# Performance work log

Measured on AMD Instinct MI355X. Metric: run time of the kernel, lower is better.

The kernel has to match this reference:

```python
import jax, jax.numpy as jnp
import numpy as np

NUM_TOKENS = 14
DIM = 128
B, N = 8, 128
NUM_ROUNDS = 5


def setup_inputs() -> dict:
    key = jax.random.key(0)
    ks = jax.random.split(key, 10)
    s = 1.0 / np.sqrt(DIM)
    return {
        "tok": jax.random.randint(ks[0], (B, N), 0, NUM_TOKENS),
        "A": jax.random.uniform(ks[1], (B, N, N), dtype=jnp.float32),
        "embed": jax.random.normal(ks[2], (NUM_TOKENS, DIM), dtype=jnp.float32),
        "W1": jax.random.normal(ks[3], (DIM, 2 * DIM), dtype=jnp.float32) * s,
        "b1": jax.random.normal(ks[4], (DIM,), dtype=jnp.float32) * s,
        "W2": jax.random.normal(ks[5], (DIM, DIM), dtype=jnp.float32) * s,
        "b2": jax.random.normal(ks[6], (DIM,), dtype=jnp.float32) * s,
        "Wo1": jax.random.normal(ks[7], (DIM, DIM), dtype=jnp.float32) * s,
        "bo1": jax.random.normal(ks[8], (DIM,), dtype=jnp.float32) * s,
        "Wo2": jax.random.normal(ks[9], (10, DIM), dtype=jnp.float32) * s,
    }


def reference(tok, A, embed, W1, b1, W2, b2, Wo1, bo1, Wo2):
    # Dropout is identity (eval mode / inference reference).
    x = embed[tok]  # [B, N, D]
    d = x.shape[-1]
    # fc1 on concat(x_i, x_j) decomposes into two per-node projections:
    # fc1([x_i, x_j]) = x_i @ W1a^T + x_j @ W1b^T + b1
    W1a, W1b = W1[:, :d], W1[:, d:]
    A_t = jnp.swapaxes(A, 1, 2)  # A.transpose(1, 2)
    for _ in range(NUM_ROUNDS):
        hi = jnp.einsum("bnd,ed->bne", x, W1a)
        hj = jnp.einsum("bnd,ed->bne", x, W1b)
        # pairwise edge MLP: [B, N, N, D]
        h = jax.nn.relu(hi[:, :, None, :] + hj[:, None, :, :] + b1)
        m = jax.nn.relu(jnp.einsum("bijd,ed->bije", h, W2) + b2)
        # mask by transposed adjacency and sum over neighbors j (axis 2)
        msg = jnp.einsum("bij,bije->bie", A_t, m)
        x = x + msg
    def head(z):
        return jax.nn.relu(z @ Wo1.T + bo1) @ Wo2.T
    out = head(x[:, 0, :])                       # [B, 10]
    x_all = head(x.reshape(-1, d)).reshape(x.shape[0], x.shape[1], 10)
    return (out, x_all)
```

## Files before the change

### kernel.cpp

```cpp
#include <hip/hip_runtime.h>
#include <hip/hip_bf16.h>

#define BB 8
#define NN 128
#define DD 128

typedef __attribute__((ext_vector_type(8))) short bf16x8;
typedef __attribute__((ext_vector_type(4))) float floatx4;
typedef __attribute__((ext_vector_type(2))) float floatx2;

__device__ __forceinline__ unsigned short f2bf(float f) {
    unsigned int bits = __float_as_uint(f);
    unsigned int r = bits + 0x7FFFu + ((bits >> 16) & 1u);
    return (unsigned short)(r >> 16);
}

__device__ __forceinline__ unsigned short f2bf_hw(float f) {
    unsigned int r;
    asm("v_cvt_pk_bf16_f32 %0, %1, %2" : "=v"(r) : "v"(f), "v"(f));
    return (unsigned short)r;
}

__device__ __forceinline__ unsigned int f2bf_pk(float lo, float hi) {
    unsigned int r;
    asm("v_cvt_pk_bf16_f32 %0, %1, %2" : "=v"(r) : "v"(lo), "v"(hi));
    return r;
}

#define WS_X16A 0
#define WS_X16B 65536
#define WS_W1T  131072
#define WS_W2B  148480
#define WS_CNT  157184

__global__ __launch_bounds__(256) void k_init(const int* __restrict__ tok,
                                              const float* __restrict__ embf,
                                              const float* __restrict__ W1f,
                                              const float* __restrict__ W2f,
                                              float* __restrict__ ws) {
    unsigned int* x16 = (unsigned int*)(ws + WS_X16A);
    unsigned short* gw1t = (unsigned short*)(ws + WS_W1T);
    unsigned short* gw2b = (unsigned short*)(ws + WS_W2B);
    int* cnt = (int*)(ws + WS_CNT);
    int blk = blockIdx.x, t = threadIdx.x;
    if (blk < 16) {
        int base = blk * 4096;
#pragma unroll
        for (int it = 0; it < 16; ++it) {
            int w = base + it * 256 + t;
            int r = w >> 6, d2 = (w & 63) * 2;
            const float* er = embf + tok[r] * DD;
            x16[w] = (unsigned int)f2bf(er[d2]) | ((unsigned int)f2bf(er[d2 + 1]) << 16);
        }
    } else if (blk < 25) {
        int base = (blk - 16) * 4096;
#pragma unroll
        for (int it = 0; it < 16; ++it) {
            int idx = base + it * 256 + t;
            if (idx < 256 * 136) {
                int e = idx / 136, d = idx - e * 136;
                gw1t[idx] = (d < 128) ? f2bf(W1f[(e & 127) * 256 + (e >> 7) * 128 + d])
                                      : (unsigned short)0;
            }
        }
    } else if (blk < 30) {
        int base = (blk - 25) * 4096;
#pragma unroll
        for (int it = 0; it < 16; ++it) {
            int idx = base + it * 256 + t;
            if (idx < 128 * 136) {
                int e = idx / 136, d = idx - e * 136;
                gw2b[idx] = (d < 128) ? f2bf(W2f[e * 128 + d]) : (unsigned short)0;
            }
        }
    } else if (blk == 30) {
#pragma unroll
        for (int it = 0; it < 4; ++it) cnt[it * 256 + t] = 0;
    }
}

__global__ __launch_bounds__(512, 2) void k_main(const int* __restrict__ tokp,
                                                 const float* __restrict__ embf,
                                                 const float* __restrict__ Af,
                                                 const float* __restrict__ b1f,
                                                 const float* __restrict__ b2f,
                                                 const float* __restrict__ Wo1f,
                                                 const float* __restrict__ bo1f,
                                                 const float* __restrict__ Wo2f,
                                                 float* __restrict__ ws,
                                                 float* __restrict__ outp) {
    __shared__ __align__(16) unsigned short w1t[256 * 136];
    __shared__ __align__(16) unsigned short w2b[128 * 136];
    __shared__ __align__(16) unsigned short xb[128 * 136];
    __shared__ __align__(16) float red[4][4][128];
    __shared__ __align__(16) float zs[4][128];
    __shared__ float a_s[4][128];
    __shared__ __align__(16) float hja_s[4][128];
    __shared__ float b1s[128], b2s[128];

    const unsigned short* gw1t = (const unsigned short*)(ws + WS_W1T);
    const unsigned short* gw2b = (const unsigned short*)(ws + WS_W2B);
    int* cnt = (int*)(ws + WS_CNT);

    int blk = blockIdx.x;
    int b = blk & 7, g = blk >> 3, i0 = g * 4;
    int t = threadIdx.x;
    int wave = t >> 6, lane = t & 63;
    int col = lane & 15, quad = lane >> 4;

    {
        const uint4* s1 = (const uint4*)gw1t; uint4* d1 = (uint4*)w1t;
#pragma unroll
        for (int it = 0; it < 9; ++it) { int idx = it * 512 + t; if (idx < 4352) d1[idx] = s1[idx]; }
        const uint4* s2 = (const uint4*)gw2b; uint4* d2 = (uint4*)w2b;
#pragma unroll
        for (int it = 0; it < 5; ++it) { int idx = it * 512 + t; if (idx < 2176) d2[idx] = s2[idx]; }
    }
    if (t < 128) { b1s[t] = b1f[t]; b2s[t] = b2f[t]; }
    a_s[t >> 7][t & 127] = Af[(b * NN + (t & 127)) * NN + i0 + (t >> 7)];

    float xown = embf[tokp[b * NN + i0 + (t >> 7)] * DD + (t & 127)];

    const int myw = g >> 2;
    const int qr  = g & 3;

    __syncthreads();

    for (int r = 0; r < 5; ++r) {
        const unsigned short* cur16 = (const unsigned short*)(ws + ((r & 1) ? WS_X16B : WS_X16A));
        unsigned short* nxt16 = (unsigned short*)(ws + ((r & 1) ? WS_X16A : WS_X16B));

        {
            const bf16x8* gp = reinterpret_cast<const bf16x8*>(
                cur16 + (size_t)(b * NN + wave * 16) * DD);
            bf16x8 v0, v1, v2, v3;
            const bf16x8* pl = gp + lane;
            asm volatile(
                "global_load_dwordx4 %0, %4, off sc0 sc1\n\t"
                "global_load_dwordx4 %1, %4, off offset:1024 sc0 sc1\n\t"
                "global_load_dwordx4 %2, %4, off offset:2048 sc0 sc1\n\t"
                "global_load_dwordx4 %3, %4, off offset:3072 sc0 sc1\n\t"
                "s_waitcnt vmcnt(0)"
                : "=&v"(v0), "=&v"(v1), "=&v"(v2), "=&v"(v3)
                : "v"(pl)
                : "memory");
            int r16 = lane >> 4, c8 = (lane & 15) * 8;
            *reinterpret_cast<bf16x8*>(&xb[(wave * 16 + r16     ) * 136 + c8]) = v0;
            *reinterpret_cast<bf16x8*>(&xb[(wave * 16 + r16 + 4 ) * 136 + c8]) = v1;
            *reinterpret_cast<bf16x8*>(&xb[(wave * 16 + r16 + 8 ) * 136 + c8]) = v2;
            *reinterpret_cast<bf16x8*>(&xb[(wave * 16 + r16 + 12) * 136 + c8]) = v3;
            __threadfence_block();
        }

        bf16x8 af[4];
#pragma unroll
        for (int ks = 0; ks < 4; ++ks)
            af[ks] = *reinterpret_cast<const bf16x8*>(&xb[(wave * 16 + col) * 136 + ks * 32 + quad * 8]);
        floatx4 acc1[16];
#pragma unroll
        for (int nt = 8; nt < 16; ++nt) acc1[nt] = (floatx4){0.f, 0.f, 0.f, 0.f};
#pragma unroll
        for (int nt = 8; nt < 16; ++nt)
#pragma unroll
            for (int ks = 0; ks < 4; ++ks) {
                bf16x8 bfc = *reinterpret_cast<const bf16x8*>(&w1t[(nt * 16 + col) * 136 + ks * 32 + quad * 8]);
                acc1[nt] = __builtin_amdgcn_mfma_f32_16x16x32_bf16(af[ks], bfc, acc1[nt], 0, 0, 0);
            }
        if (wave == myw) {
#pragma unroll
            for (int nt = 0; nt < 8; ++nt) acc1[nt] = (floatx4){0.f, 0.f, 0.f, 0.f};
#pragma unroll
            for (int nt = 0; nt < 8; ++nt)
#pragma unroll
                for (int ks = 0; ks < 4; ++ks) {
                    bf16x8 bfc = *reinterpret_cast<const bf16x8*>(&w1t[(nt * 16 + col) * 136 + ks * 32 + quad * 8]);
                    acc1[nt] = __builtin_amdgcn_mfma_f32_16x16x32_bf16(af[ks], bfc, acc1[nt], 0, 0, 0);
                }
            if (quad == qr) {
#pragma unroll
                for (int nt = 0; nt < 8; ++nt) {
                    int d = nt * 16 + col;
#pragma unroll
                    for (int rr = 0; rr < 4; ++rr) hja_s[rr][d] = acc1[nt][rr];
                }
            }
        }
#pragma unroll
        for (int nt = 8; nt < 16; ++nt) {
            int d = (nt - 8) * 16 + col;
#pragma unroll
            for (int rr = 0; rr < 4; ++rr) {
                int j = wave * 16 + quad * 4 + rr;
                xb[j * 136 + d] = f2bf_hw(acc1[nt][rr] + b1s[d]);
            }
        }
        __syncthreads();

        int we = wave & 1, wj = wave >> 1;
        int ebase = we * 64, jbase = wj * 32;
        bf16x8 bw[4][4];
#pragma unroll
        for (int et = 0; et < 4; ++et)
#pragma unroll
            for (int ks = 0; ks < 4; ++ks)
                bw[et][ks] = *reinterpret_cast<const bf16x8*>(&w2b[(ebase + et * 16 + col) * 136 + ks * 32 + quad * 8]);

        floatx2 hjc[2][4][4];
#pragma unroll
        for (int jt = 0; jt < 2; ++jt)
#pragma unroll
            for (int ks = 0; ks < 4; ++ks) {
                union { bf16x8 v; unsigned int u[4]; } Rw;
                Rw.v = *reinterpret_cast<const bf16x8*>(&xb[(jbase + jt * 16 + col) * 136 + ks * 32 + quad * 8]);
#pragma unroll
                for (int p = 0; p < 4; ++p) {
                    floatx2 h2;
                    h2.x = __uint_as_float(Rw.u[p] << 16);
                    h2.y = __uint_as_float(Rw.u[p] & 0xFFFF0000u);
                    hjc[jt][ks][p] = h2;
                }
            }

#pragma unroll
        for (int ii = 0; ii < 4; ++ii) {
            floatx4 acc2[2][4];
#pragma unroll
            for (int jt = 0; jt < 2; ++jt)
#pragma unroll
                for (int et = 0; et < 4; ++et) acc2[jt][et] = (floatx4){0.f, 0.f, 0.f, 0.f};
#pragma unroll
            for (int ks = 0; ks < 4; ++ks) {
                int k0 = ks * 32 + quad * 8;
                floatx2 ha[4];
#pragma unroll
                for (int p = 0; p < 4; ++p)
                    ha[p] = *reinterpret_cast<const floatx2*>(&hja_s[ii][k0 + 2 * p]);
#pragma unroll
                for (int jt = 0; jt < 2; ++jt) {
                    union { bf16x8 v; unsigned int u[4]; } Ho;
#pragma unroll
                    for (int p = 0; p < 4; ++p) {
                        floatx2 s2;
                        asm("v_pk_add_f32 %0, %1, %2" : "=v"(s2) : "v"(hjc[jt][ks][p]), "v"(ha[p]));
                        float f0 = fmaxf(s2.x, 0.f);
                        float f1 = fmaxf(s2.y, 0.f);
                        Ho.u[p] = f2bf_pk(f0, f1);
                    }
#pragma unroll
                    for (int et = 0; et < 4; ++et)
                        acc2[jt][et] = __builtin_amdgcn_mfma_f32_16x16x32_bf16(Ho.v, bw[et][ks], acc2[jt][et], 0, 0, 0);
                }
            }
#pragma unroll
            for (int et = 0; et < 4; ++et) {
                int e = ebase + et * 16 + col;
                float be = b2s[e];
                float s = 0.f;
#pragma unroll
                for (int jt = 0; jt < 2; ++jt) {
                    int j0 = jbase + jt * 16 + quad * 4;
#pragma unroll
                    for (int rr = 0; rr < 4; ++rr)
                        s += a_s[ii][j0 + rr] * fmaxf(acc2[jt][et][rr] + be, 0.f);
                }
                s += __shfl_xor(s, 16, 64);
                s += __shfl_xor(s, 32, 64);
                if (quad == 0) red[wj][ii][e] = s;
            }
        }
        __syncthreads();
        {
            int ii = t >> 7, e = t & 127;
            float msg = red[0][ii][e] + red[1][ii][e] + red[2][ii][e] + red[3][ii][e];
            xown += msg;
            if (r < 4) {
                float po = __shfl_xor(xown, 1, 64);
                if ((e & 1) == 0) {
                    unsigned int pk = f2bf_pk(xown, po);
                    unsigned int* dst = (unsigned int*)nxt16 + (((b * NN + i0 + ii) * DD + e) >> 1);
                    __hip_atomic_store(dst, pk, __ATOMIC_RELAXED, __HIP_MEMORY_SCOPE_AGENT);
                }
            } else {
                zs[ii][e] = xown;
            }
        }
        if (r < 4) {
            __atomic_signal_fence(__ATOMIC_SEQ_CST);
            __builtin_amdgcn_s_waitcnt(0);
            __syncthreads();
            if (t == 0) {
                int* myc = cnt + (b * 4 + r) * 32;
                __hip_atomic_fetch_add(myc, 1, __ATOMIC_RELAXED, __HIP_MEMORY_SCOPE_AGENT);
                while (__hip_atomic_load(myc, __ATOMIC_RELAXED, __HIP_MEMORY_SCOPE_AGENT) < 32)
                    __builtin_amdgcn_s_sleep(1);
            }
            __syncthreads();
        } else {
            __syncthreads();
        }
    }

    float* wo1s = (float*)w1t;
#pragma unroll
    for (int it = 0; it < 8; ++it) {
        int idx4 = it * 512 + t;
        int e = idx4 >> 5, d4 = idx4 & 31;
        float4 wv = reinterpret_cast<const float4*>(Wo1f)[idx4];
        *reinterpret_cast<float4*>(&wo1s[e * 136 + d4 * 4]) = wv;
    }
    __syncthreads();
    {
        int ii = t >> 7, e = t & 127;
        float acc = 0.f;
#pragma unroll
        for (int d4 = 0; d4 < 32; ++d4) {
            float4 w = *reinterpret_cast<const float4*>(&wo1s[e * 136 + d4 * 4]);
            float4 z = *reinterpret_cast<const float4*>(&zs[ii][d4 * 4]);
            acc += w.x * z.x + w.y * z.y + w.z * z.z + w.w * z.w;
        }
        ((float*)red)[ii * 128 + e] = fmaxf(acc + bo1f[e], 0.f);
    }
    __syncthreads();
    if (t < 40) {
        int ii = t / 10, o = t - ii * 10;
        const float* rsrow = (const float*)red + ii * 128;
        const float4* w2r = reinterpret_cast<const float4*>(Wo2f + o * DD);
        float s = 0.f;
#pragma unroll
        for (int e4 = 0; e4 < 32; ++e4) {
            float4 rv = *reinterpret_cast<const float4*>(&rsrow[e4 * 4]);
            float4 wv = w2r[e4];
            s += rv.x * wv.x + rv.y * wv.y + rv.z * wv.z + rv.w * wv.w;
        }
        int row = b * NN + i0 + ii;
        outp[80 + row * 10 + o] = s;
        if (i0 + ii == 0) outp[b * 10 + o] = s;
    }
}

extern "C" void kernel_launch(void* const* d_in, const int* in_sizes, int n_in,
                              void* d_out, int out_size, void* d_ws, size_t ws_size,
                              hipStream_t stream) {
    const int*   tok  = (const int*)d_in[0];
    const float* Af   = (const float*)d_in[1];
    const float* embf = (const float*)d_in[2];
    const float* W1f  = (const float*)d_in[3];
    const float* b1f  = (const float*)d_in[4];
    const float* W2f  = (const float*)d_in[5];
    const float* b2f  = (const float*)d_in[6];
    const float* Wo1f = (const float*)d_in[7];
    const float* bo1f = (const float*)d_in[8];
    const float* Wo2f = (const float*)d_in[9];

    float* ws  = (float*)d_ws;
    float* out = (float*)d_out;

    k_init<<<31, 256, 0, stream>>>(tok, embf, W1f, W2f, ws);
    k_main<<<256, 512, 0, stream>>>(tok, embf, Af, b1f, b2f, Wo1f, bo1f, Wo2f, ws, out);
}
```

Baseline: 144.8 us.

## Exchange hj projections instead of node states and precompute round-0 token tables

Each block now computes the W1a/W1b projections only for its own four nodes and publishes the bf16 hj rows to global memory. Previously every block reloaded all 128 node states and recomputed the full hj projection redundantly each round. Round 0 reads hj and hi from per-token tables that k_init builds with MFMA over the 14 embeddings, so the first grid barrier disappears. This removes redundant per-block GEMM work and a large LDS staging buffer. In exchange, the inter-block barrier moves to the start of each later round and hj is rounded to bf16 after the bias is added.

```diff
diff --git a/kernel.cpp b/kernel.cpp
--- a/kernel.cpp
+++ b/kernel.cpp
@@ -1,7 +1,6 @@
 #include <hip/hip_runtime.h>
 #include <hip/hip_bf16.h>
 
-#define BB 8
 #define NN 128
 #define DD 128
 
@@ -27,33 +26,81 @@
     return r;
 }
 
-#define WS_X16A 0
-#define WS_X16B 65536
+#define WS_HJB0 0
+#define WS_HJB1 65536
 #define WS_W1T  131072
 #define WS_W2B  148480
-#define WS_CNT  157184
+#define WS_TABA 157184
+#define WS_TABB 158976
+#define WS_CNT  159872
 
 __global__ __launch_bounds__(256) void k_init(const int* __restrict__ tok,
                                               const float* __restrict__ embf,
                                               const float* __restrict__ W1f,
+                                              const float* __restrict__ b1f,
                                               const float* __restrict__ W2f,
                                               float* __restrict__ ws) {
-    unsigned int* x16 = (unsigned int*)(ws + WS_X16A);
     unsigned short* gw1t = (unsigned short*)(ws + WS_W1T);
     unsigned short* gw2b = (unsigned short*)(ws + WS_W2B);
+    float* taba = ws + WS_TABA;
+    unsigned int* tabb32 = (unsigned int*)(ws + WS_TABB);
     int* cnt = (int*)(ws + WS_CNT);
     int blk = blockIdx.x, t = threadIdx.x;
-    if (blk < 16) {
-        int base = blk * 4096;
-#pragma unroll
-        for (int it = 0; it < 16; ++it) {
-            int w = base + it * 256 + t;
-            int r = w >> 6, d2 = (w & 63) * 2;
-            const float* er = embf + tok[r] * DD;
-            x16[w] = (unsigned int)f2bf(er[d2]) | ((unsigned int)f2bf(er[d2 + 1]) << 16);
-        }
-    } else if (blk < 25) {
-        int base = (blk - 16) * 4096;
+
+    if (blk == 0) {
+        __shared__ __align__(16) unsigned short wt[256 * 136];
+        __shared__ __align__(16) unsigned short et_[16 * 136];
+        __shared__ float b1s[128];
+        for (int idx = t; idx < 256 * 136; idx += 256) {
+            int e = idx / 136, d = idx - e * 136;
+            wt[idx] = (d < 128) ? f2bf(W1f[(e & 127) * 256 + (e >> 7) * 128 + d])
+                                : (unsigned short)0;
+        }
+        for (int i = t; i < 16 * 136; i += 256) et_[i] = 0;
+        if (t < 128) b1s[t] = b1f[t];
+        __syncthreads();
+        if (t < 224) {
+            int v = t >> 4, d0 = (t & 15) * 8;
+#pragma unroll
+            for (int k2 = 0; k2 < 8; ++k2) et_[v * 136 + d0 + k2] = f2bf(embf[v * 128 + d0 + k2]);
+        }
+        __syncthreads();
+        int wv = t >> 6, lane = t & 63, col = lane & 15, quad = lane >> 4;
+        bf16x8 af[4];
+#pragma unroll
+        for (int ks = 0; ks < 4; ++ks)
+            af[ks] = *reinterpret_cast<const bf16x8*>(&et_[col * 136 + ks * 32 + quad * 8]);
+#pragma unroll
+        for (int c = 0; c < 4; ++c) {
+            int nt = wv * 4 + c;
+            floatx4 acc = (floatx4){0.f, 0.f, 0.f, 0.f};
+#pragma unroll
+            for (int ks = 0; ks < 4; ++ks)
+                acc = __builtin_amdgcn_mfma_f32_16x16x32_bf16(af[ks],
+                        *reinterpret_cast<const bf16x8*>(&wt[(nt * 16 + col) * 136 + ks * 32 + quad * 8]),
+                        acc, 0, 0, 0);
+            if (nt < 8) {
+#pragma unroll
+                for (int rr = 0; rr < 4; ++rr) {
+                    int v = quad * 4 + rr;
+                    if (v < 14) taba[v * 128 + nt * 16 + col] = acc[rr];
+                }
+            } else {
+                int d = (nt - 8) * 16 + col;
+                float bv = b1s[d];
+#pragma unroll
+                for (int rr = 0; rr < 4; ++rr) {
+                    float val = acc[rr] + bv;
+                    float po = __shfl_xor(val, 1, 64);
+                    int v = quad * 4 + rr;
+                    if (!(col & 1) && v < 14)
+                        tabb32[v * 64 + (d >> 1)] =
+                            (unsigned int)f2bf(val) | ((unsigned int)f2bf(po) << 16);
+                }
+            }
+        }
+    } else if (blk < 10) {
+        int base = (blk - 1) * 4096;
 #pragma unroll
         for (int it = 0; it < 16; ++it) {
             int idx = base + it * 256 + t;
@@ -63,8 +110,8 @@
                                       : (unsigned short)0;
             }
         }
-    } else if (blk < 30) {
-        int base = (blk - 25) * 4096;
+    } else if (blk < 15) {
+        int base = (blk - 10) * 4096;
 #pragma unroll
         for (int it = 0; it < 16; ++it) {
             int idx = base + it * 256 + t;
@@ -73,7 +120,7 @@
                 gw2b[idx] = (d < 128) ? f2bf(W2f[e * 128 + d]) : (unsigned short)0;
             }
         }
-    } else if (blk == 30) {
+    } else {
 #pragma unroll
         for (int it = 0; it < 4; ++it) cnt[it * 256 + t] = 0;
     }
@@ -91,15 +138,16 @@
                                                  float* __restrict__ outp) {
     __shared__ __align__(16) unsigned short w1t[256 * 136];
     __shared__ __align__(16) unsigned short w2b[128 * 136];
-    __shared__ __align__(16) unsigned short xb[128 * 136];
+    __shared__ __align__(16) unsigned short xo[4 * 136];
     __shared__ __align__(16) float red[4][4][128];
     __shared__ __align__(16) float zs[4][128];
     __shared__ float a_s[4][128];
     __shared__ __align__(16) float hja_s[4][128];
-    __shared__ float b1s[128], b2s[128];
 
     const unsigned short* gw1t = (const unsigned short*)(ws + WS_W1T);
     const unsigned short* gw2b = (const unsigned short*)(ws + WS_W2B);
+    const float* taba = ws + WS_TABA;
+    const unsigned short* tabb16 = (const unsigned short*)(ws + WS_TABB);
     int* cnt = (int*)(ws + WS_CNT);
 
     int blk = blockIdx.x;
@@ -116,110 +164,132 @@
 #pragma unroll
         for (int it = 0; it < 5; ++it) { int idx = it * 512 + t; if (idx < 2176) d2[idx] = s2[idx]; }
     }
-    if (t < 128) { b1s[t] = b1f[t]; b2s[t] = b2f[t]; }
+    int we = wave & 1, wj = wave >> 1;
+    int ebase = we * 64, jbase = wj * 32;
+    float b1r0 = 0.f, b1r1 = 0.f;
+    if (wave >= 4) {
+        b1r0 = b1f[((wave - 4) * 2 + 0) * 16 + col];
+        b1r1 = b1f[((wave - 4) * 2 + 1) * 16 + col];
+    }
+    float b2r[4];
+#pragma unroll
+    for (int et = 0; et < 4; ++et) b2r[et] = b2f[ebase + et * 16 + col];
     a_s[t >> 7][t & 127] = Af[(b * NN + (t & 127)) * NN + i0 + (t >> 7)];
 
-    float xown = embf[tokp[b * NN + i0 + (t >> 7)] * DD + (t & 127)];
-
-    const int myw = g >> 2;
-    const int qr  = g & 3;
-
+    int ii_own = t >> 7, e_own = t & 127;
+    int trow = tokp[b * NN + i0 + ii_own];
+    float xown = embf[trow * DD + e_own];
+    hja_s[ii_own][e_own] = taba[trow * 128 + e_own];
     __syncthreads();
 
     for (int r = 0; r < 5; ++r) {
-        const unsigned short* cur16 = (const unsigned short*)(ws + ((r & 1) ? WS_X16B : WS_X16A));
-        unsigned short* nxt16 = (unsigned short*)(ws + ((r & 1) ? WS_X16A : WS_X16B));
-
+        unsigned short* gbw = (unsigned short*)(ws + ((r & 1) ? WS_HJB1 : WS_HJB0));
+
+        if (r > 0) {
+            bf16x8 af[4];
+#pragma unroll
+            for (int ks = 0; ks < 4; ++ks) {
+                bf16x8 z = {0, 0, 0, 0, 0, 0, 0, 0};
+                af[ks] = (col < 4) ? *reinterpret_cast<const bf16x8*>(&xo[col * 136 + ks * 32 + quad * 8]) : z;
+            }
+            floatx4 acc[2];
+            acc[0] = (floatx4){0.f, 0.f, 0.f, 0.f};
+            acc[1] = (floatx4){0.f, 0.f, 0.f, 0.f};
+#pragma unroll
+            for (int u = 0; u < 2; ++u)
+#pragma unroll
+                for (int ks = 0; ks < 4; ++ks) {
+                    int nt = wave * 2 + u;
+                    acc[u] = __builtin_amdgcn_mfma_f32_16x16x32_bf16(af[ks],
+                        *reinterpret_cast<const bf16x8*>(&w1t[(nt * 16 + col) * 136 + ks * 32 + quad * 8]),
+                        acc[u], 0, 0, 0);
+                }
+            if (wave < 4) {
+                if (quad == 0) {
+#pragma unroll
+                    for (int u = 0; u < 2; ++u)
+#pragma unroll
+                        for (int rr = 0; rr < 4; ++rr)
+                            hja_s[rr][(wave * 2 + u) * 16 + col] = acc[u][rr];
+                }
+            } else {
+#pragma unroll
+                for (int u = 0; u < 2; ++u) {
+                    float bv = u ? b1r1 : b1r0;
+                    int d = ((wave - 4) * 2 + u) * 16 + col;
+#pragma unroll
+                    for (int rr = 0; rr < 4; ++rr) {
+                        float val = acc[u][rr] + bv;
+                        float po = __shfl_xor(val, 1, 64);
+                        if (quad == 0 && !(col & 1)) {
+                            int row = b * NN + i0 + rr;
+                            __hip_atomic_store((unsigned int*)gbw + row * 64 + (d >> 1),
+                                               f2bf_pk(val, po),
+                                               __ATOMIC_RELAXED, __HIP_MEMORY_SCOPE_AGENT);
+                        }
+                    }
+                }
+            }
+            __atomic_signal_fence(__ATOMIC_SEQ_CST);
+            __builtin_amdgcn_s_waitcnt(0);
+            __syncthreads();
+            if (t == 0) {
+                int* myc = cnt + (b * 4 + (r - 1)) * 32;
+                __hip_atomic_fetch_add(myc, 1, __ATOMIC_RELAXED, __HIP_MEMORY_SCOPE_AGENT);
+                while (__hip_atomic_load(myc, __ATOMIC_RELAXED, __HIP_MEMORY_SCOPE_AGENT) < 32)
+                    __builtin_amdgcn_s_sleep(1);
+            }
+            __syncthreads();
+        }
+
+        union U4 { bf16x8 v; unsigned int u[4]; };
+        U4 L[2][4];
         {
-            const bf16x8* gp = reinterpret_cast<const bf16x8*>(
-                cur16 + (size_t)(b * NN + wave * 16) * DD);
-            bf16x8 v0, v1, v2, v3;
-            const bf16x8* pl = gp + lane;
+            const unsigned short* base0;
+            const unsigned short* base1;
+            if (r == 0) {
+                base0 = tabb16 + (size_t)tokp[b * NN + jbase + col] * 128;
+                base1 = tabb16 + (size_t)tokp[b * NN + jbase + 16 + col] * 128;
+            } else {
+                base0 = gbw + (size_t)(b * NN + jbase + col) * 128;
+                base1 = gbw + (size_t)(b * NN + jbase + 16 + col) * 128;
+            }
+            base0 += quad * 8; base1 += quad * 8;
             asm volatile(
-                "global_load_dwordx4 %0, %4, off sc0 sc1\n\t"
-                "global_load_dwordx4 %1, %4, off offset:1024 sc0 sc1\n\t"
-                "global_load_dwordx4 %2, %4, off offset:2048 sc0 sc1\n\t"
-                "global_load_dwordx4 %3, %4, off offset:3072 sc0 sc1\n\t"
-                "s_waitcnt vmcnt(0)"
-                : "=&v"(v0), "=&v"(v1), "=&v"(v2), "=&v"(v3)
-                : "v"(pl)
+                "global_load_dwordx4 %0, %8, off sc0 sc1\n\t"
+                "global_load_dwordx4 %1, %8, off offset:64 sc0 sc1\n\t"
+                "global_load_dwordx4 %2, %8, off offset:128 sc0 sc1\n\t"
+                "global_load_dwordx4 %3, %8, off offset:192 sc0 sc1\n\t"
+                "global_load_dwordx4 %4, %9, off sc0 sc1\n\t"
+                "global_load_dwordx4 %5, %9, off offset:64 sc0 sc1\n\t"
+                "global_load_dwordx4 %6, %9, off offset:128 sc0 sc1\n\t"
+                "global_load_dwordx4 %7, %9, off offset:192 sc0 sc1"
+                : "=&v"(L[0][0].v), "=&v"(L[0][1].v), "=&v"(L[0][2].v), "=&v"(L[0][3].v),
+                  "=&v"(L[1][0].v), "=&v"(L[1][1].v), "=&v"(L[1][2].v), "=&v"(L[1][3].v)
+                : "v"(base0), "v"(base1)
                 : "memory");
-            int r16 = lane >> 4, c8 = (lane & 15) * 8;
-            *reinterpret_cast<bf16x8*>(&xb[(wave * 16 + r16     ) * 136 + c8]) = v0;
-            *reinterpret_cast<bf16x8*>(&xb[(wave * 16 + r16 + 4 ) * 136 + c8]) = v1;
-            *reinterpret_cast<bf16x8*>(&xb[(wave * 16 + r16 + 8 ) * 136 + c8]) = v2;
-            *reinterpret_cast<bf16x8*>(&xb[(wave * 16 + r16 + 12) * 136 + c8]) = v3;
-            __threadfence_block();
-        }
-
-        bf16x8 af[4];
-#pragma unroll
-        for (int ks = 0; ks < 4; ++ks)
-            af[ks] = *reinterpret_cast<const bf16x8*>(&xb[(wave * 16 + col) * 136 + ks * 32 + quad * 8]);
-        floatx4 acc1[16];
-#pragma unroll
-        for (int nt = 8; nt < 16; ++nt) acc1[nt] = (floatx4){0.f, 0.f, 0.f, 0.f};
-#pragma unroll
-        for (int nt = 8; nt < 16; ++nt)
-#pragma unroll
-            for (int ks = 0; ks < 4; ++ks) {
-                bf16x8 bfc = *reinterpret_cast<const bf16x8*>(&w1t[(nt * 16 + col) * 136 + ks * 32 + quad * 8]);
-                acc1[nt] = __builtin_amdgcn_mfma_f32_16x16x32_bf16(af[ks], bfc, acc1[nt], 0, 0, 0);
-            }
-        if (wave == myw) {
-#pragma unroll
-            for (int nt = 0; nt < 8; ++nt) acc1[nt] = (floatx4){0.f, 0.f, 0.f, 0.f};
-#pragma unroll
-            for (int nt = 0; nt < 8; ++nt)
-#pragma unroll
-                for (int ks = 0; ks < 4; ++ks) {
-                    bf16x8 bfc = *reinterpret_cast<const bf16x8*>(&w1t[(nt * 16 + col) * 136 + ks * 32 + quad * 8]);
-                    acc1[nt] = __builtin_amdgcn_mfma_f32_16x16x32_bf16(af[ks], bfc, acc1[nt], 0, 0, 0);
-                }
-            if (quad == qr) {
-#pragma unroll
-                for (int nt = 0; nt < 8; ++nt) {
-                    int d = nt * 16 + col;
-#pragma unroll
-                    for (int rr = 0; rr < 4; ++rr) hja_s[rr][d] = acc1[nt][rr];
-                }
-            }
-        }
-#pragma unroll
-        for (int nt = 8; nt < 16; ++nt) {
-            int d = (nt - 8) * 16 + col;
-#pragma unroll
-            for (int rr = 0; rr < 4; ++rr) {
-                int j = wave * 16 + quad * 4 + rr;
-                xb[j * 136 + d] = f2bf_hw(acc1[nt][rr] + b1s[d]);
-            }
-        }
-        __syncthreads();
-
-        int we = wave & 1, wj = wave >> 1;
-        int ebase = we * 64, jbase = wj * 32;
+        }
         bf16x8 bw[4][4];
 #pragma unroll
         for (int et = 0; et < 4; ++et)
 #pragma unroll
             for (int ks = 0; ks < 4; ++ks)
                 bw[et][ks] = *reinterpret_cast<const bf16x8*>(&w2b[(ebase + et * 16 + col) * 136 + ks * 32 + quad * 8]);
+        asm volatile("s_waitcnt vmcnt(0)" ::: "memory");
+        __builtin_amdgcn_sched_barrier(0);
 
         floatx2 hjc[2][4][4];
 #pragma unroll
         for (int jt = 0; jt < 2; ++jt)
 #pragma unroll
-            for (int ks = 0; ks < 4; ++ks) {
-                union { bf16x8 v; unsigned int u[4]; } Rw;
-                Rw.v = *reinterpret_cast<const bf16x8*>(&xb[(jbase + jt * 16 + col) * 136 + ks * 32 + quad * 8]);
+            for (int ks = 0; ks < 4; ++ks)
 #pragma unroll
                 for (int p = 0; p < 4; ++p) {
                     floatx2 h2;
-                    h2.x = __uint_as_float(Rw.u[p] << 16);
-                    h2.y = __uint_as_float(Rw.u[p] & 0xFFFF0000u);
+                    h2.x = __uint_as_float(L[jt][ks].u[p] << 16);
+                    h2.y = __uint_as_float(L[jt][ks].u[p] & 0xFFFF0000u);
                     hjc[jt][ks][p] = h2;
                 }
-            }
 
 #pragma unroll
         for (int ii = 0; ii < 4; ++ii) {
@@ -237,7 +307,7 @@
                     ha[p] = *reinterpret_cast<const floatx2*>(&hja_s[ii][k0 + 2 * p]);
 #pragma unroll
                 for (int jt = 0; jt < 2; ++jt) {
-                    union { bf16x8 v; unsigned int u[4]; } Ho;
+                    U4 Ho;
 #pragma unroll
                     for (int p = 0; p < 4; ++p) {
                         floatx2 s2;
@@ -253,8 +323,7 @@
             }
 #pragma unroll
             for (int et = 0; et < 4; ++et) {
-                int e = ebase + et * 16 + col;
-                float be = b2s[e];
+                float be = b2r[et];
                 float s = 0.f;
 #pragma unroll
                 for (int jt = 0; jt < 2; ++jt) {
@@ -265,39 +334,18 @@
                 }
                 s += __shfl_xor(s, 16, 64);
                 s += __shfl_xor(s, 32, 64);
-                if (quad == 0) red[wj][ii][e] = s;
+                if (quad == 0) red[wj][ii][ebase + et * 16 + col] = s;
             }
         }
         __syncthreads();
         {
-            int ii = t >> 7, e = t & 127;
-            float msg = red[0][ii][e] + red[1][ii][e] + red[2][ii][e] + red[3][ii][e];
+            float msg = red[0][ii_own][e_own] + red[1][ii_own][e_own]
+                      + red[2][ii_own][e_own] + red[3][ii_own][e_own];
             xown += msg;
-            if (r < 4) {
-                float po = __shfl_xor(xown, 1, 64);
-                if ((e & 1) == 0) {
-                    unsigned int pk = f2bf_pk(xown, po);
-                    unsigned int* dst = (unsigned int*)nxt16 + (((b * NN + i0 + ii) * DD + e) >> 1);
-                    __hip_atomic_store(dst, pk, __ATOMIC_RELAXED, __HIP_MEMORY_SCOPE_AGENT);
-                }
-            } else {
-                zs[ii][e] = xown;
-            }
-        }
-        if (r < 4) {
-            __atomic_signal_fence(__ATOMIC_SEQ_CST);
-            __builtin_amdgcn_s_waitcnt(0);
-            __syncthreads();
-            if (t == 0) {
-                int* myc = cnt + (b * 4 + r) * 32;
-                __hip_atomic_fetch_add(myc, 1, __ATOMIC_RELAXED, __HIP_MEMORY_SCOPE_AGENT);
-                while (__hip_atomic_load(myc, __ATOMIC_RELAXED, __HIP_MEMORY_SCOPE_AGENT) < 32)
-                    __builtin_amdgcn_s_sleep(1);
-            }
-            __syncthreads();
-        } else {
-            __syncthreads();
-        }
+            if (r < 4) xo[ii_own * 136 + e_own] = f2bf_hw(xown);
+            else       zs[ii_own][e_own] = xown;
+        }
+        if (r < 4) __syncthreads();
     }
 
     float* wo1s = (float*)w1t;
@@ -310,7 +358,7 @@
     }
     __syncthreads();
     {
-        int ii = t >> 7, e = t & 127;
+        int e = t & 127, ii = t >> 7;
         float acc = 0.f;
 #pragma unroll
         for (int d4 = 0; d4 < 32; ++d4) {
@@ -355,6 +403,6 @@
     float* ws  = (float*)d_ws;
     float* out = (float*)d_out;
 
-    k_init<<<31, 256, 0, stream>>>(tok, embf, W1f, W2f, ws);
+    k_init<<<16, 256, 0, stream>>>(tok, embf, W1f, b1f, W2f, ws);
     k_main<<<256, 512, 0, stream>>>(tok, embf, Af, b1f, b2f, Wo1f, bo1f, Wo2f, ws, out);
 }
```

After: 172.2 us. +18.9%, slower.
